# Optimization experiments

Hardware: AMD Instinct MI355X
Metric: run time of the kernel (lower is better)

## Reference

```python
import jax, jax.numpy as jnp
import numpy as np

B, C, N = 16, 64, 2048
K, KS, OC = 20, 20, 64
BN_EPS = 1e-5


def setup_inputs() -> dict:
    key = jax.random.key(0)
    k1, k2, k3, k4 = jax.random.split(key, 4)
    feature = jax.random.normal(k1, (B, C, N), dtype=jnp.float32)
    neigh_indexs = jax.random.randint(k2, (B * N, K), 0, B * N, dtype=jnp.int64)
    permatrix = jax.random.normal(k3, (B * N, K, KS), dtype=jnp.float32)
    conv_w = jax.random.normal(k4, (OC, 2 * C), dtype=jnp.float32) * 0.05  # 1x1 conv weight
    conv_b = jnp.zeros((OC,), dtype=jnp.float32)
    gamma = jnp.ones((OC,), dtype=jnp.float32)
    beta = jnp.zeros((OC,), dtype=jnp.float32)
    return {"feature": feature, "neigh_indexs": neigh_indexs, "permatrix": permatrix,
            "conv_w": conv_w, "conv_b": conv_b, "gamma": gamma, "beta": beta}


def _forward(feature, neigh_indexs, permatrix, conv_w, conv_b, gamma, beta):
    bsize, num_feat, num_pts = feature.shape
    # [B, C, N] -> [B*N, C]
    flat = jnp.transpose(feature, (0, 2, 1)).reshape(bsize * num_pts, num_feat)
    # neighbor gather: [B*N, K, C] -> [B*N, C, K]
    feats = jnp.transpose(flat[neigh_indexs], (0, 2, 1))
    f_repeat = jnp.broadcast_to(feats[:, :, 0:1], feats.shape)
    f_relative = feats - f_repeat
    feats = jnp.concatenate([f_repeat, f_relative], axis=1)  # [B*N, 2C, K]
    # per-point small matmul with permutation matrix: [B*N, 2C, KS]
    feats = jnp.einsum('nck,nks->ncs', feats, permatrix)
    # 1x1 conv over channel dim: [B*N, OC, KS]
    out = jnp.einsum('ncs,oc->nos', feats, conv_w) + conv_b[None, :, None]
    # max over neighbors, reshape to [B, OC, N]
    out = jnp.max(out, axis=-1).reshape(bsize, num_pts, -1)
    out = jnp.transpose(out, (0, 2, 1))  # [B, OC, N]
    # BatchNorm1d (training-mode forward: biased var over batch & points)
    mean = jnp.mean(out, axis=(0, 2), keepdims=True)
    var = jnp.var(out, axis=(0, 2), keepdims=True)
    out = (out - mean) * jax.lax.rsqrt(var + BN_EPS)
    return out * gamma[None, :, None] + beta[None, :, None]


def reference(feature, neigh_indexs, permatrix, conv_w, conv_b, gamma, beta):
    return _forward(feature, neigh_indexs, permatrix, conv_w, conv_b, gamma, beta)
```

## Files before the change

kernel.cpp:

```cpp
#include <hip/hip_runtime.h>

#define B_   16
#define C_   64
#define N_   2048
#define M_   (B_ * N_)
#define K_   20
#define KS_  20
#define OC_  64
#define NWAVE2 8192

__device__ __forceinline__ void load_lds16(const float* g, float* l) {
    __builtin_amdgcn_global_load_lds(
        (const __attribute__((address_space(1))) void*)g,
        (__attribute__((address_space(3))) void*)l, 16, 0, 0);
}

__global__ __launch_bounds__(256) void k_project(
    const float* __restrict__ feat,
    const float* __restrict__ conv_w,
    float* __restrict__ pq)
{
    const int lane = threadIdx.x & 63;
    const int wg   = blockIdx.x * 4 + (threadIdx.x >> 6);
    float w2[64], wd[64];
    const float4* cw4 = (const float4*)conv_w;
    #pragma unroll
    for (int j = 0; j < 16; ++j) {
        float4 a = cw4[lane * 32 + j];
        float4 b = cw4[lane * 32 + 16 + j];
        w2[4*j+0] = b.x; w2[4*j+1] = b.y; w2[4*j+2] = b.z; w2[4*j+3] = b.w;
        wd[4*j+0] = a.x - b.x; wd[4*j+1] = a.y - b.y;
        wd[4*j+2] = a.z - b.z; wd[4*j+3] = a.w - b.w;
    }
    const int m0 = wg * 16;
    int b0 = m0 >> 11, p0 = m0 & 2047;
    float fv = feat[((size_t)(b0 * 64 + lane)) * 2048 + p0];
    for (int mi = 0; mi < 16; ++mi) {
        const int m = m0 + mi;
        float fnext = 0.f;
        if (mi < 15) {
            const int mn = m + 1;
            fnext = feat[((size_t)((mn >> 11) * 64 + lane)) * 2048 + (mn & 2047)];
        }
        float p0a = 0.f, p1a = 0.f, q0a = 0.f, q1a = 0.f;
        #pragma unroll
        for (int c = 0; c < 32; ++c) {
            float f0 = __int_as_float(
                __builtin_amdgcn_readlane(__float_as_int(fv), c));
            float f1 = __int_as_float(
                __builtin_amdgcn_readlane(__float_as_int(fv), c + 32));
            p0a = fmaf(w2[c], f0, p0a);
            p1a = fmaf(w2[c + 32], f1, p1a);
            q0a = fmaf(wd[c], f0, q0a);
            q1a = fmaf(wd[c + 32], f1, q1a);
        }
        pq[(size_t)m * 128 + lane]      = p0a + p1a;
        pq[(size_t)m * 128 + 64 + lane] = q0a + q1a;
        fv = fnext;
    }
}

__global__ __launch_bounds__(256) void k_points(
    const float* __restrict__ pq,
    const int*   __restrict__ nidx,
    const float* __restrict__ perm,
    const float* __restrict__ conv_b,
    float* __restrict__ pre,
    float* __restrict__ partials)
{
    __shared__ float plds[4 * 2 * 400];
    const int tid  = threadIdx.x;
    const int lane = tid & 63;
    const int w    = __builtin_amdgcn_readfirstlane(tid >> 6);
    const int wg   = __builtin_amdgcn_readfirstlane((int)blockIdx.x * 4 + w);
    float* mybuf = &plds[w * 800];

    const float bias = conv_b[lane];
    float sum = 0.f, sumsq = 0.f;

    {
        const float* src = perm + (size_t)wg * 400;
        load_lds16(src + lane * 4, mybuf);
        if (lane < 36) load_lds16(src + 256 + lane * 4, mybuf + 256);
    }
    int iv = 0;
    if (lane < 20) iv = nidx[(size_t)wg * K_ + lane];

    #pragma unroll
    for (int it = 0; it < 4; ++it) {
        const int n = wg + NWAVE2 * it;
        float* cur = mybuf + (it & 1) * 400;
        int ik[20];
        #pragma unroll
        for (int k = 0; k < 20; ++k) ik[k] = __builtin_amdgcn_readlane(iv, k);
        float q = pq[(size_t)ik[0] * 128 + 64 + lane];
        float pk[20];
        #pragma unroll
        for (int k = 0; k < 20; ++k) pk[k] = pq[(size_t)ik[k] * 128 + lane];
        if (it < 3) {
            const int nn = n + NWAVE2;
            if (lane < 20) iv = nidx[(size_t)nn * K_ + lane];
            const float* src = perm + (size_t)nn * 400;
            float* nxt = mybuf + ((it + 1) & 1) * 400;
            load_lds16(src + lane * 4, nxt);
            if (lane < 36) load_lds16(src + 256 + lane * 4, nxt + 256);
        }
        if (it < 3) __builtin_amdgcn_s_waitcnt(0x0F74);
        else        __builtin_amdgcn_s_waitcnt(0x0F70);
        __asm__ volatile("" ::: "memory");

        float acc[20];
        #pragma unroll
        for (int s = 0; s < 20; ++s) acc[s] = bias;
        #pragma unroll
        for (int k = 0; k < 20; ++k) {
            const float t = pk[k] + q;
            const float4* pr = (const float4*)(cur + k * 20);
            float4 a0 = pr[0], a1 = pr[1], a2 = pr[2], a3 = pr[3], a4 = pr[4];
            acc[ 0] = fmaf(t, a0.x, acc[ 0]); acc[ 1] = fmaf(t, a0.y, acc[ 1]);
            acc[ 2] = fmaf(t, a0.z, acc[ 2]); acc[ 3] = fmaf(t, a0.w, acc[ 3]);
            acc[ 4] = fmaf(t, a1.x, acc[ 4]); acc[ 5] = fmaf(t, a1.y, acc[ 5]);
            acc[ 6] = fmaf(t, a1.z, acc[ 6]); acc[ 7] = fmaf(t, a1.w, acc[ 7]);
            acc[ 8] = fmaf(t, a2.x, acc[ 8]); acc[ 9] = fmaf(t, a2.y, acc[ 9]);
            acc[10] = fmaf(t, a2.z, acc[10]); acc[11] = fmaf(t, a2.w, acc[11]);
            acc[12] = fmaf(t, a3.x, acc[12]); acc[13] = fmaf(t, a3.y, acc[13]);
            acc[14] = fmaf(t, a3.z, acc[14]); acc[15] = fmaf(t, a3.w, acc[15]);
            acc[16] = fmaf(t, a4.x, acc[16]); acc[17] = fmaf(t, a4.y, acc[17]);
            acc[18] = fmaf(t, a4.z, acc[18]); acc[19] = fmaf(t, a4.w, acc[19]);
        }
        float mv = acc[0];
        #pragma unroll
        for (int s = 1; s < 20; ++s) mv = fmaxf(mv, acc[s]);
        pre[(size_t)n * 64 + lane] = mv;
        sum += mv;
        sumsq = fmaf(mv, mv, sumsq);
    }
    partials[(size_t)wg * 128 + lane]      = sum;
    partials[(size_t)wg * 128 + 64 + lane] = sumsq;
}

__global__ __launch_bounds__(256) void k_stats(
    const float* __restrict__ partials,
    const float* __restrict__ gamma,
    const float* __restrict__ beta,
    float* __restrict__ stats)
{
    const int ch  = blockIdx.x;
    const int tid = threadIdx.x;
    double s = 0.0, s2 = 0.0;
    for (int w = tid; w < NWAVE2; w += 256) {
        s  += (double)partials[(size_t)w * 128 + ch];
        s2 += (double)partials[(size_t)w * 128 + 64 + ch];
    }
    __shared__ double sh_s[256];
    __shared__ double sh_q[256];
    sh_s[tid] = s; sh_q[tid] = s2;
    __syncthreads();
    for (int off = 128; off > 0; off >>= 1) {
        if (tid < off) { sh_s[tid] += sh_s[tid + off]; sh_q[tid] += sh_q[tid + off]; }
        __syncthreads();
    }
    if (tid == 0) {
        const double inv_n = 1.0 / (double)M_;
        double mean = sh_s[0] * inv_n;
        double var  = sh_q[0] * inv_n - mean * mean;
        double inv  = 1.0 / sqrt(var + 1e-5);
        double sc   = (double)gamma[ch] * inv;
        stats[ch]      = (float)sc;
        stats[64 + ch] = (float)((double)beta[ch] - mean * sc);
    }
}

__global__ __launch_bounds__(256) void k_apply(
    const float* __restrict__ pre,
    const float* __restrict__ stats,
    float* __restrict__ out)
{
    __shared__ float tile[64 * 65];
    __shared__ float scl[64];
    __shared__ float shf[64];
    const int tid = threadIdx.x;
    if (tid < 64)       scl[tid]      = stats[tid];
    else if (tid < 128) shf[tid - 64] = stats[tid];
    __syncthreads();
    const int b  = blockIdx.x >> 5;
    const int pt = (blockIdx.x & 31) * 64;
    const int c  = tid & 63;
    const int r0 = tid >> 6;
    #pragma unroll
    for (int i = 0; i < 16; ++i) {
        const int r = i * 4 + r0;
        float v = pre[((size_t)(b * 2048 + pt + r)) * 64 + c];
        tile[c * 65 + r] = fmaf(v, scl[c], shf[c]);
    }
    __syncthreads();
    #pragma unroll
    for (int i = 0; i < 16; ++i) {
        const int o = i * 4 + r0;
        out[((size_t)(b * 64 + o)) * 2048 + pt + c] = tile[o * 65 + c];
    }
}

extern "C" void kernel_launch(void* const* d_in, const int* in_sizes, int n_in,
                              void* d_out, int out_size, void* d_ws, size_t ws_size,
                              hipStream_t stream) {
    const float* feat   = (const float*)d_in[0];
    const int*   nidx   = (const int*)  d_in[1];
    const float* perm   = (const float*)d_in[2];
    const float* conv_w = (const float*)d_in[3];
    const float* conv_b = (const float*)d_in[4];
    const float* gamma  = (const float*)d_in[5];
    const float* beta   = (const float*)d_in[6];
    float* out = (float*)d_out;

    char* ws = (char*)d_ws;
    float* pq       = (float*)ws;
    float* pre      = (float*)(ws + (size_t)M_ * 128 * 4);
    float* partials = (float*)(ws + (size_t)M_ * 128 * 4
                                  + (size_t)M_ * 64 * 4);
    float* stats    = (float*)(ws + (size_t)M_ * 128 * 4
                                  + (size_t)M_ * 64 * 4
                                  + (size_t)NWAVE2 * 128 * 4);

    hipLaunchKernelGGL(k_project, dim3(512),  dim3(256), 0, stream, feat, conv_w, pq);
    hipLaunchKernelGGL(k_points,  dim3(2048), dim3(256), 0, stream, pq, nidx, perm,
                       conv_b, pre, partials);
    hipLaunchKernelGGL(k_stats,   dim3(64),   dim3(256), 0, stream, partials, gamma,
                       beta, stats);
    hipLaunchKernelGGL(k_apply,   dim3(512),  dim3(256), 0, stream, pre, stats, out);
}
```

Before: 175.1 us.

## Keep permutation matrix in registers and broadcast via readlane instead of LDS

The k_points kernel stops staging each point's 20x20 permutation matrix in LDS through async global-to-LDS loads. Each lane now holds a float4 slice in registers and every coefficient is broadcast with readlane, with the next point's slice prefetched in a register double buffer. This removes the LDS traffic and the waitcnt synchronisation, but costs 400 readlane instructions per point and more register pressure. The per-wave statistics partials are also reduced within the block through shared memory, which cuts the work k_stats has to do.

```diff
diff --git a/kernel.cpp b/kernel.cpp
--- a/kernel.cpp
+++ b/kernel.cpp
@@ -8,12 +8,7 @@
 #define KS_  20
 #define OC_  64
 #define NWAVE2 8192
-
-__device__ __forceinline__ void load_lds16(const float* g, float* l) {
-    __builtin_amdgcn_global_load_lds(
-        (const __attribute__((address_space(1))) void*)g,
-        (__attribute__((address_space(3))) void*)l, 16, 0, 0);
-}
+#define NBLK2  2048
 
 __global__ __launch_bounds__(256) void k_project(
     const float* __restrict__ feat,
@@ -60,6 +55,67 @@
     }
 }
 
+template<int E>
+__device__ __forceinline__ float bro(const float4& pa, const float4& pb) {
+    constexpr int c = E & 3;
+    float v;
+    if constexpr (E < 256) {
+        if constexpr (c == 0) v = pa.x; else if constexpr (c == 1) v = pa.y;
+        else if constexpr (c == 2) v = pa.z; else v = pa.w;
+    } else {
+        if constexpr (c == 0) v = pb.x; else if constexpr (c == 1) v = pb.y;
+        else if constexpr (c == 2) v = pb.z; else v = pb.w;
+    }
+    constexpr int l = (E < 256) ? (E >> 2) : ((E >> 2) - 64);
+    return __int_as_float(__builtin_amdgcn_readlane(__float_as_int(v), l));
+}
+
+#define KS1(K,S) acc[S] = fmaf(t, bro<(K)*20+(S)>(pa, pb), acc[S]);
+#define KSTEP(K) { const float t = pk[K] + q; \
+    KS1(K,0)  KS1(K,1)  KS1(K,2)  KS1(K,3)  KS1(K,4)  \
+    KS1(K,5)  KS1(K,6)  KS1(K,7)  KS1(K,8)  KS1(K,9)  \
+    KS1(K,10) KS1(K,11) KS1(K,12) KS1(K,13) KS1(K,14) \
+    KS1(K,15) KS1(K,16) KS1(K,17) KS1(K,18) KS1(K,19) }
+
+template<bool PREF>
+__device__ __forceinline__ void point_step(
+    int n, int lane, float bias, int& iv,
+    float4& pa, float4& pb, float4& npa, float4& npb,
+    const float* __restrict__ pq, const int* __restrict__ nidx,
+    const float* __restrict__ perm,
+    float* __restrict__ pre, float& sum, float& sumsq)
+{
+    int ik[20];
+    #pragma unroll
+    for (int k = 0; k < 20; ++k) ik[k] = __builtin_amdgcn_readlane(iv, k);
+    float q = pq[(size_t)ik[0] * 128 + 64 + lane];
+    float pk[20];
+    #pragma unroll
+    for (int k = 0; k < 20; ++k) pk[k] = pq[(size_t)ik[k] * 128 + lane];
+    if (PREF) {
+        const int nn = n + NWAVE2;
+        if (lane < 20) iv = nidx[(size_t)nn * K_ + lane];
+        const float* src = perm + (size_t)nn * 400;
+        npa = *(const float4*)(src + lane * 4);
+        if (lane < 36) npb = *(const float4*)(src + 256 + lane * 4);
+    }
+
+    float acc[20];
+    #pragma unroll
+    for (int s = 0; s < 20; ++s) acc[s] = bias;
+    KSTEP(0)  KSTEP(1)  KSTEP(2)  KSTEP(3)  KSTEP(4)
+    KSTEP(5)  KSTEP(6)  KSTEP(7)  KSTEP(8)  KSTEP(9)
+    KSTEP(10) KSTEP(11) KSTEP(12) KSTEP(13) KSTEP(14)
+    KSTEP(15) KSTEP(16) KSTEP(17) KSTEP(18) KSTEP(19)
+
+    float mv = acc[0];
+    #pragma unroll
+    for (int s = 1; s < 20; ++s) mv = fmaxf(mv, acc[s]);
+    pre[(size_t)n * 64 + lane] = mv;
+    sum += mv;
+    sumsq = fmaf(mv, mv, sumsq);
+}
+
 __global__ __launch_bounds__(256) void k_points(
     const float* __restrict__ pq,
     const int*   __restrict__ nidx,
@@ -68,76 +124,44 @@
     float* __restrict__ pre,
     float* __restrict__ partials)
 {
-    __shared__ float plds[4 * 2 * 400];
     const int tid  = threadIdx.x;
     const int lane = tid & 63;
-    const int w    = __builtin_amdgcn_readfirstlane(tid >> 6);
-    const int wg   = __builtin_amdgcn_readfirstlane((int)blockIdx.x * 4 + w);
-    float* mybuf = &plds[w * 800];
+    const int w    = tid >> 6;
+    const int wg   = (int)blockIdx.x * 4 + w;
 
     const float bias = conv_b[lane];
     float sum = 0.f, sumsq = 0.f;
 
+    float4 pa, pb, npa, npb;
+    int iv = 0;
     {
         const float* src = perm + (size_t)wg * 400;
-        load_lds16(src + lane * 4, mybuf);
-        if (lane < 36) load_lds16(src + 256 + lane * 4, mybuf + 256);
-    }
-    int iv = 0;
-    if (lane < 20) iv = nidx[(size_t)wg * K_ + lane];
-
-    #pragma unroll
-    for (int it = 0; it < 4; ++it) {
-        const int n = wg + NWAVE2 * it;
-        float* cur = mybuf + (it & 1) * 400;
-        int ik[20];
-        #pragma unroll
-        for (int k = 0; k < 20; ++k) ik[k] = __builtin_amdgcn_readlane(iv, k);
-        float q = pq[(size_t)ik[0] * 128 + 64 + lane];
-        float pk[20];
-        #pragma unroll
-        for (int k = 0; k < 20; ++k) pk[k] = pq[(size_t)ik[k] * 128 + lane];
-        if (it < 3) {
-            const int nn = n + NWAVE2;
-            if (lane < 20) iv = nidx[(size_t)nn * K_ + lane];
-            const float* src = perm + (size_t)nn * 400;
-            float* nxt = mybuf + ((it + 1) & 1) * 400;
-            load_lds16(src + lane * 4, nxt);
-            if (lane < 36) load_lds16(src + 256 + lane * 4, nxt + 256);
-        }
-        if (it < 3) __builtin_amdgcn_s_waitcnt(0x0F74);
-        else        __builtin_amdgcn_s_waitcnt(0x0F70);
-        __asm__ volatile("" ::: "memory");
-
-        float acc[20];
-        #pragma unroll
-        for (int s = 0; s < 20; ++s) acc[s] = bias;
-        #pragma unroll
-        for (int k = 0; k < 20; ++k) {
-            const float t = pk[k] + q;
-            const float4* pr = (const float4*)(cur + k * 20);
-            float4 a0 = pr[0], a1 = pr[1], a2 = pr[2], a3 = pr[3], a4 = pr[4];
-            acc[ 0] = fmaf(t, a0.x, acc[ 0]); acc[ 1] = fmaf(t, a0.y, acc[ 1]);
-            acc[ 2] = fmaf(t, a0.z, acc[ 2]); acc[ 3] = fmaf(t, a0.w, acc[ 3]);
-            acc[ 4] = fmaf(t, a1.x, acc[ 4]); acc[ 5] = fmaf(t, a1.y, acc[ 5]);
-            acc[ 6] = fmaf(t, a1.z, acc[ 6]); acc[ 7] = fmaf(t, a1.w, acc[ 7]);
-            acc[ 8] = fmaf(t, a2.x, acc[ 8]); acc[ 9] = fmaf(t, a2.y, acc[ 9]);
-            acc[10] = fmaf(t, a2.z, acc[10]); acc[11] = fmaf(t, a2.w, acc[11]);
-            acc[12] = fmaf(t, a3.x, acc[12]); acc[13] = fmaf(t, a3.y, acc[13]);
-            acc[14] = fmaf(t, a3.z, acc[14]); acc[15] = fmaf(t, a3.w, acc[15]);
-            acc[16] = fmaf(t, a4.x, acc[16]); acc[17] = fmaf(t, a4.y, acc[17]);
-            acc[18] = fmaf(t, a4.z, acc[18]); acc[19] = fmaf(t, a4.w, acc[19]);
-        }
-        float mv = acc[0];
-        #pragma unroll
-        for (int s = 1; s < 20; ++s) mv = fmaxf(mv, acc[s]);
-        pre[(size_t)n * 64 + lane] = mv;
-        sum += mv;
-        sumsq = fmaf(mv, mv, sumsq);
-    }
-    partials[(size_t)wg * 128 + lane]      = sum;
-    partials[(size_t)wg * 128 + 64 + lane] = sumsq;
-}
+        pa = *(const float4*)(src + lane * 4);
+        if (lane < 36) pb = *(const float4*)(src + 256 + lane * 4);
+        if (lane < 20) iv = nidx[(size_t)wg * K_ + lane];
+    }
+
+    point_step<true >(wg,              lane, bias, iv, pa,  pb,  npa, npb,
+                      pq, nidx, perm, pre, sum, sumsq);
+    point_step<true >(wg + NWAVE2,     lane, bias, iv, npa, npb, pa,  pb,
+                      pq, nidx, perm, pre, sum, sumsq);
+    point_step<true >(wg + 2 * NWAVE2, lane, bias, iv, pa,  pb,  npa, npb,
+                      pq, nidx, perm, pre, sum, sumsq);
+    point_step<false>(wg + 3 * NWAVE2, lane, bias, iv, npa, npb, pa,  pb,
+                      pq, nidx, perm, pre, sum, sumsq);
+
+    __shared__ float red[512];
+    red[w * 128 + lane]      = sum;
+    red[w * 128 + 64 + lane] = sumsq;
+    __syncthreads();
+    if (tid < 128) {
+        float s = red[tid] + red[128 + tid] + red[256 + tid] + red[384 + tid];
+        partials[(size_t)blockIdx.x * 128 + tid] = s;
+    }
+}
+
+#undef KSTEP
+#undef KS1
 
 __global__ __launch_bounds__(256) void k_stats(
     const float* __restrict__ partials,
@@ -148,7 +172,7 @@
     const int ch  = blockIdx.x;
     const int tid = threadIdx.x;
     double s = 0.0, s2 = 0.0;
-    for (int w = tid; w < NWAVE2; w += 256) {
+    for (int w = tid; w < NBLK2; w += 256) {
         s  += (double)partials[(size_t)w * 128 + ch];
         s2 += (double)partials[(size_t)w * 128 + 64 + ch];
     }
@@ -220,7 +244,7 @@
                                   + (size_t)M_ * 64 * 4);
     float* stats    = (float*)(ws + (size_t)M_ * 128 * 4
                                   + (size_t)M_ * 64 * 4
-                                  + (size_t)NWAVE2 * 128 * 4);
+                                  + (size_t)NBLK2 * 128 * 4);
 
     hipLaunchKernelGGL(k_project, dim3(512),  dim3(256), 0, stream, feat, conv_w, pq);
     hipLaunchKernelGGL(k_points,  dim3(2048), dim3(256), 0, stream, pq, nidx, perm,
```

Measured after the change: 181.6 us. 3.7% more time.
